# Optimization experiments

Hardware: AMD Instinct MI355X
Metric: run time of the kernel (lower is better)

## Reference

```python
import jax, jax.numpy as jnp
import numpy as np

TOKENS, IN_F, OUT_F = 8192, 4096, 4096


def setup_inputs() -> dict:
    key = jax.random.key(0)
    k1, k2 = jax.random.split(key)
    return {
        "input": jax.random.normal(k1, (TOKENS, IN_F), dtype=jnp.float32),
        "weight": jax.random.normal(k2, (OUT_F, IN_F), dtype=jnp.float32),
        "weight_scale": jnp.ones((1,), dtype=jnp.float32),
        "input_scale": jnp.ones((1,), dtype=jnp.float32),
    }


def reference(input, weight, weight_scale, input_scale):
    # BitNet-style: ternary weight quantization {-1, 0, +1} w.r.t. learned scale,
    # int8-range activation quantization, fused dequant-scaled matmul.
    ws = weight_scale[0]
    xs = input_scale[0]
    # quantize_weights: round(w / ws) clipped to ternary
    w_q = jnp.clip(jnp.round(weight / ws), -1.0, 1.0)          # [out, in], values in {-1,0,1}
    # fused_quantize_matmul: quantize activations to int8 range, matmul, dequant scale
    x_q = jnp.clip(jnp.round(input / xs), -128.0, 127.0)        # [tokens, in]
    out = jnp.einsum('ti,oi->to', x_q, w_q) * (xs * ws)         # [tokens, out]
    return out
```

## Files before the change

### kernel.cpp

```cpp
#include <hip/hip_runtime.h>
#include <hip/hip_bf16.h>
#include <stdint.h>


typedef int  int4v  __attribute__((ext_vector_type(4)));
typedef int  int16v __attribute__((ext_vector_type(16)));

typedef __attribute__((address_space(1))) void gvoid;
typedef __attribute__((address_space(3))) void lvoid;

#define M_DIM 8192
#define N_DIM 4096
#define K_DIM 4096

#define BM 128
#define BN 128
#define BK 128

__global__ __launch_bounds__(256) void quant_kernel(
    const float* __restrict__ in, int8_t* __restrict__ out,
    const float* __restrict__ scale_ptr, float lo, float hi, long n) {
  long i = ((long)blockIdx.x * blockDim.x + threadIdx.x) * 16;
  if (i >= n) return;
  float s = scale_ptr[0];
  float4 a = *(const float4*)(in + i);
  float4 b = *(const float4*)(in + i + 4);
  float4 c = *(const float4*)(in + i + 8);
  float4 d = *(const float4*)(in + i + 12);
  float v[16] = {a.x, a.y, a.z, a.w, b.x, b.y, b.z, b.w,
                 c.x, c.y, c.z, c.w, d.x, d.y, d.z, d.w};
  union { int8_t c[16]; int4 q; } u;
#pragma unroll
  for (int t = 0; t < 16; ++t) {
    float q = rintf(v[t] / s);
    q = fminf(fmaxf(q, lo), hi);
    u.c[t] = (int8_t)q;
  }
  *(int4*)(out + i) = u.q;
}

__global__ __launch_bounds__(256) void gemm_bt(
    const int8_t* __restrict__ A,
    const int8_t* __restrict__ B,
    float* __restrict__ C,
    const float* __restrict__ ws_ptr, const float* __restrict__ xs_ptr) {
  __shared__ __attribute__((aligned(16))) char smem[2 * BM * BK];
  char* sA = smem;
  char* sB = smem + BM * BK;

  const int tid  = threadIdx.x;
  const int wave = tid >> 6;
  const int lane = tid & 63;
  const int wr   = wave >> 1;
  const int wc   = wave & 1;
  const int r    = lane & 31;
  const int half = lane >> 5;

  const long m0 = (long)blockIdx.y * BM;
  const long n0 = (long)blockIdx.x * BN;

  const int srow   = wave * 32 + (lane >> 3);
  const int schunk = ((lane & 7) ^ (lane >> 3)) * 16;
  const int8_t* gA = A + (m0 + srow) * K_DIM + schunk;
  const int8_t* gB = B + (n0 + srow) * K_DIM + schunk;
  char* lA = sA + wave * 4096;
  char* lB = sB + wave * 4096;

  int16v acc[2][2] = {};

  for (int k0 = 0; k0 < K_DIM; k0 += BK) {
#pragma unroll
    for (int t = 0; t < 4; ++t)
      __builtin_amdgcn_global_load_lds((gvoid*)(gA + t * 8 * K_DIM),
                                       (lvoid*)(lA + t * 1024), 16, 0, 0);
#pragma unroll
    for (int t = 0; t < 4; ++t)
      __builtin_amdgcn_global_load_lds((gvoid*)(gB + t * 8 * K_DIM),
                                       (lvoid*)(lB + t * 1024), 16, 0, 0);
    gA += BK;
    gB += BK;
    __syncthreads();

    const int arow = (wr * 64 + r) * BK;
    const int brow = (wc * 64 + r) * BK;
#pragma unroll
    for (int ks = 0; ks < 4; ++ks) {
      const int co = (((ks * 2 + half) ^ (lane & 7)) * 16);
      int4v a0 = *(const int4v*)(sA + arow + co);
      int4v a1 = *(const int4v*)(sA + arow + 32 * BK + co);
      int4v b0 = *(const int4v*)(sB + brow + co);
      int4v b1 = *(const int4v*)(sB + brow + 32 * BK + co);
      acc[0][0] = __builtin_amdgcn_mfma_i32_32x32x32_i8(a0, b0, acc[0][0], 0, 0, 0);
      acc[0][1] = __builtin_amdgcn_mfma_i32_32x32x32_i8(a0, b1, acc[0][1], 0, 0, 0);
      acc[1][0] = __builtin_amdgcn_mfma_i32_32x32x32_i8(a1, b0, acc[1][0], 0, 0, 0);
      acc[1][1] = __builtin_amdgcn_mfma_i32_32x32x32_i8(a1, b1, acc[1][1], 0, 0, 0);
    }

    __syncthreads();
  }

  const float s = ws_ptr[0] * xs_ptr[0];
#pragma unroll
  for (int mb = 0; mb < 2; ++mb) {
#pragma unroll
    for (int nb = 0; nb < 2; ++nb) {
      const long col = n0 + wc * 64 + nb * 32 + r;
      const long rowbase = m0 + wr * 64 + mb * 32 + 4 * half;
#pragma unroll
      for (int reg = 0; reg < 16; ++reg) {
        const long row = rowbase + (reg & 3) + 8 * (reg >> 2);
        C[row * N_DIM + col] = (float)acc[mb][nb][reg] * s;
      }
    }
  }
}

extern "C" void kernel_launch(void* const* d_in, const int* in_sizes, int n_in,
                              void* d_out, int out_size, void* d_ws, size_t ws_size,
                              hipStream_t stream) {
  const float* x  = (const float*)d_in[0];
  const float* w  = (const float*)d_in[1];
  const float* ws = (const float*)d_in[2];
  const float* xs = (const float*)d_in[3];
  float* out = (float*)d_out;

  int8_t* xq = (int8_t*)d_ws;
  int8_t* wq = (int8_t*)d_ws + (size_t)M_DIM * K_DIM;

  const long n_x = (long)M_DIM * K_DIM;
  const long n_w = (long)N_DIM * K_DIM;

  quant_kernel<<<(n_x / 16 + 255) / 256, 256, 0, stream>>>(x, xq, xs, -128.f, 127.f, n_x);
  quant_kernel<<<(n_w / 16 + 255) / 256, 256, 0, stream>>>(w, wq, ws, -1.f, 1.f, n_w);

  dim3 grid(N_DIM / BN, M_DIM / BM);
  gemm_bt<<<grid, 256, 0, stream>>>(xq, wq, out, ws, xs);
}
```

Before: 389.8 us.

## Enlarge GEMM block tile to 256x128 with 4x2 MFMA tiles per wave

Doubles the M dimension of the block tile so each wave computes a 128x64 output region with eight 32x32 int8 MFMA accumulators. The aim is to raise arithmetic intensity per LDS load and per global fetch, and to halve the number of blocks that reload the B tile. In exchange each thread holds twice the accumulator registers and the block uses 48KB of LDS, which can lower occupancy; launch_bounds now requests 2 blocks per CU.

```diff
diff --git a/kernel.cpp b/kernel.cpp
--- a/kernel.cpp
+++ b/kernel.cpp
@@ -13,7 +13,7 @@
 #define N_DIM 4096
 #define K_DIM 4096
 
-#define BM 128
+#define BM 256
 #define BN 128
 #define BK 128
 
@@ -39,12 +39,12 @@
   *(int4*)(out + i) = u.q;
 }
 
-__global__ __launch_bounds__(256) void gemm_bt(
+__global__ __launch_bounds__(256, 2) void gemm_bt(
     const int8_t* __restrict__ A,
     const int8_t* __restrict__ B,
     float* __restrict__ C,
     const float* __restrict__ ws_ptr, const float* __restrict__ xs_ptr) {
-  __shared__ __attribute__((aligned(16))) char smem[2 * BM * BK];
+  __shared__ __attribute__((aligned(16))) char smem[BM * BK + BN * BK];
   char* sA = smem;
   char* sB = smem + BM * BK;
 
@@ -59,18 +59,18 @@
   const long m0 = (long)blockIdx.y * BM;
   const long n0 = (long)blockIdx.x * BN;
 
-  const int srow   = wave * 32 + (lane >> 3);
-  const int schunk = ((lane & 7) ^ (lane >> 3)) * 16;
-  const int8_t* gA = A + (m0 + srow) * K_DIM + schunk;
-  const int8_t* gB = B + (n0 + srow) * K_DIM + schunk;
-  char* lA = sA + wave * 4096;
+  const int lrow   = lane >> 3;
+  const int schunk = ((lane & 7) ^ lrow) * 16;
+  const int8_t* gA = A + (m0 + wave * 64 + lrow) * K_DIM + schunk;
+  const int8_t* gB = B + (n0 + wave * 32 + lrow) * K_DIM + schunk;
+  char* lA = sA + wave * 8192;
   char* lB = sB + wave * 4096;
 
-  int16v acc[2][2] = {};
+  int16v acc[4][2] = {};
 
   for (int k0 = 0; k0 < K_DIM; k0 += BK) {
 #pragma unroll
-    for (int t = 0; t < 4; ++t)
+    for (int t = 0; t < 8; ++t)
       __builtin_amdgcn_global_load_lds((gvoid*)(gA + t * 8 * K_DIM),
                                        (lvoid*)(lA + t * 1024), 16, 0, 0);
 #pragma unroll
@@ -81,19 +81,21 @@
     gB += BK;
     __syncthreads();
 
-    const int arow = (wr * 64 + r) * BK;
-    const int brow = (wc * 64 + r) * BK;
 #pragma unroll
     for (int ks = 0; ks < 4; ++ks) {
       const int co = (((ks * 2 + half) ^ (lane & 7)) * 16);
-      int4v a0 = *(const int4v*)(sA + arow + co);
-      int4v a1 = *(const int4v*)(sA + arow + 32 * BK + co);
-      int4v b0 = *(const int4v*)(sB + brow + co);
-      int4v b1 = *(const int4v*)(sB + brow + 32 * BK + co);
-      acc[0][0] = __builtin_amdgcn_mfma_i32_32x32x32_i8(a0, b0, acc[0][0], 0, 0, 0);
-      acc[0][1] = __builtin_amdgcn_mfma_i32_32x32x32_i8(a0, b1, acc[0][1], 0, 0, 0);
-      acc[1][0] = __builtin_amdgcn_mfma_i32_32x32x32_i8(a1, b0, acc[1][0], 0, 0, 0);
-      acc[1][1] = __builtin_amdgcn_mfma_i32_32x32x32_i8(a1, b1, acc[1][1], 0, 0, 0);
+      int4v af[4], bf[2];
+#pragma unroll
+      for (int mb = 0; mb < 4; ++mb)
+        af[mb] = *(const int4v*)(sA + (wr * 128 + mb * 32 + r) * BK + co);
+#pragma unroll
+      for (int nb = 0; nb < 2; ++nb)
+        bf[nb] = *(const int4v*)(sB + (wc * 64 + nb * 32 + r) * BK + co);
+#pragma unroll
+      for (int mb = 0; mb < 4; ++mb)
+#pragma unroll
+        for (int nb = 0; nb < 2; ++nb)
+          acc[mb][nb] = __builtin_amdgcn_mfma_i32_32x32x32_i8(af[mb], bf[nb], acc[mb][nb], 0, 0, 0);
     }
 
     __syncthreads();
@@ -101,11 +103,11 @@
 
   const float s = ws_ptr[0] * xs_ptr[0];
 #pragma unroll
-  for (int mb = 0; mb < 2; ++mb) {
+  for (int mb = 0; mb < 4; ++mb) {
 #pragma unroll
     for (int nb = 0; nb < 2; ++nb) {
       const long col = n0 + wc * 64 + nb * 32 + r;
-      const long rowbase = m0 + wr * 64 + mb * 32 + 4 * half;
+      const long rowbase = m0 + wr * 128 + mb * 32 + 4 * half;
 #pragma unroll
       for (int reg = 0; reg < 16; ++reg) {
         const long row = rowbase + (reg & 3) + 8 * (reg >> 2);
```

After: 393.8 us. Within noise of the previous version (+1.0%).
